# Kernel optimization log

Hardware: AMD Instinct MI355X
Metric: run time of the kernel (lower is better)

## Reference

```python
import jax, jax.numpy as jnp
import numpy as np

RADIUS = 5          # box-filter radius -> 11x11 kernel
TEMP = 0.5          # multinomial temperature
NSAMP = 5           # sampling_num
EPS = 1e-6
BN_EPS = 1e-5


def _conv(x, w, stride=1, padding=0, groups=1):
    return jax.lax.conv_general_dilated(
        x, w, window_strides=(stride, stride),
        padding=[(padding, padding), (padding, padding)],
        feature_group_count=groups,
        dimension_numbers=("NCHW", "OIHW", "NCHW"))


def custom_conv(x, w, key, stride=1, padding=0):
    """conv2d with cosine-activation regularization (bias=False path)."""
    B = x.shape[0]
    Cout = w.shape[0]
    # all-ones 'norm' conv on x*x
    x_norm = jnp.sqrt(_conv(x * x, jnp.ones_like(w), stride, padding))
    y = _conv(x, w, stride, padding)
    w_norm = jnp.sqrt(jnp.sum(w * w, axis=(1, 2, 3)))  # per-out-channel Frobenius norm
    cosine = y / (w_norm[None, :, None, None] + EPS) / (x_norm + EPS)
    # 11x11 depthwise box filter
    k = 2 * RADIUS + 1
    dw = jnp.ones((Cout, 1, k, k), x.dtype)
    cosine_mean = _conv(cosine, dw, 1, RADIUS, groups=Cout) / (k * k)
    H, W = cosine.shape[2], cosine.shape[3]
    # multinomial(NSAMP, exp(cosine/TEMP)) counts, no_grad in original
    logits = jax.lax.stop_gradient(cosine).reshape(B, Cout, H * W) / TEMP
    idx = jax.random.categorical(key, logits, axis=-1, shape=(NSAMP, B, Cout))
    bi = jnp.broadcast_to(jnp.arange(B)[None, :, None], (NSAMP, B, Cout))
    ci = jnp.broadcast_to(jnp.arange(Cout)[None, None, :], (NSAMP, B, Cout))
    mask = jnp.zeros((B, Cout, H * W), x.dtype).at[bi, ci, idx].add(1.0)
    cm = cosine_mean.reshape(B, Cout, H * W)
    act = ((mask * cm).sum(-1) / mask.sum(-1)).mean()
    return y, act


def batchnorm(x, g, b):
    # training-mode batch statistics (biased variance), like nn.BatchNorm2d
    m = x.mean(axis=(0, 2, 3), keepdims=True)
    v = x.var(axis=(0, 2, 3), keepdims=True)
    return (x - m) / jnp.sqrt(v + BN_EPS) * g[None, :, None, None] + b[None, :, None, None]


def setup_inputs() -> dict:
    key = jax.random.key(0)
    ks = jax.random.split(key, 10)
    x = jax.random.normal(ks[0], (16, 256, 56, 56), jnp.float32)
    w1 = jax.random.normal(ks[1], (64, 256, 1, 1), jnp.float32) * 0.05
    w2 = jax.random.normal(ks[2], (64, 64, 3, 3), jnp.float32) * 0.05
    w3 = jax.random.normal(ks[3], (256, 64, 1, 1), jnp.float32) * 0.05
    g1 = 1.0 + 0.05 * jax.random.normal(ks[4], (64,), jnp.float32)
    b1 = 0.05 * jax.random.normal(ks[5], (64,), jnp.float32)
    g2 = 1.0 + 0.05 * jax.random.normal(ks[6], (64,), jnp.float32)
    b2 = 0.05 * jax.random.normal(ks[7], (64,), jnp.float32)
    g3 = 1.0 + 0.05 * jax.random.normal(ks[8], (256,), jnp.float32)
    b3 = 0.05 * jax.random.normal(ks[9], (256,), jnp.float32)
    return {"x": x, "w1": w1, "w2": w2, "w3": w3,
            "g1": g1, "b1": b1, "g2": g2, "b2": b2, "g3": g3, "b3": b3}


def reference(x, w1, w2, w3, g1, b1, g2, b2, g3, b3):
    k0, k1, k2 = jax.random.split(jax.random.key(42), 3)
    acc = jnp.asarray(0.0, x.dtype)
    out, a = custom_conv(x, w1, k0)           # conv1x1
    acc = acc + a
    out = jax.nn.relu(batchnorm(out, g1, b1))
    out, a = custom_conv(out, w2, k1, padding=1)  # conv3x3, stride 1
    acc = acc + a
    out = jax.nn.relu(batchnorm(out, g2, b2))
    out, a = custom_conv(out, w3, k2)         # conv1x1 expand
    acc = acc + a
    out = batchnorm(out, g3, b3)
    out = jax.nn.relu(out + x)                # identity shortcut (downsample=None)
    return out, acc
```

## Files before the change

### kernel.cpp

```cpp
#include <hip/hip_runtime.h>
#include <stdint.h>
#include <math.h>

#define HW 3136
#define NPIX 50176

typedef __attribute__((ext_vector_type(8))) short bf16x8;
typedef __attribute__((ext_vector_type(4))) float f32x4;
#define MFMA16(a, b, c) __builtin_amdgcn_mfma_f32_16x16x32_bf16(a, b, c, 0, 0, 0)

__device__ __forceinline__ unsigned short f2bf(float f) {
  unsigned u = __float_as_uint(f);
  u = (u + 0x7fffu + ((u >> 16) & 1u)) >> 16;
  return (unsigned short)u;
}
__device__ __forceinline__ unsigned pk2(float a, float b) {
  return (unsigned)f2bf(a) | ((unsigned)f2bf(b) << 16);
}
__device__ __forceinline__ float bf2f(unsigned short h) {
  return __uint_as_float(((unsigned)h) << 16);
}

#define ROTL32(v, r) __builtin_rotateleft32((uint32_t)(v), (r))

__host__ __device__ inline void threefry2x32(uint32_t k0, uint32_t k1,
                                             uint32_t x0, uint32_t x1,
                                             uint32_t& o0, uint32_t& o1) {
  uint32_t k2 = k0 ^ k1 ^ 0x1BD11BDAu;
  x0 += k0; x1 += k1;
  x0 += x1; x1 = ROTL32(x1, 13); x1 ^= x0;
  x0 += x1; x1 = ROTL32(x1, 15); x1 ^= x0;
  x0 += x1; x1 = ROTL32(x1, 26); x1 ^= x0;
  x0 += x1; x1 = ROTL32(x1, 6);  x1 ^= x0;
  x0 += k1; x1 += k2 + 1u;
  x0 += x1; x1 = ROTL32(x1, 17); x1 ^= x0;
  x0 += x1; x1 = ROTL32(x1, 29); x1 ^= x0;
  x0 += x1; x1 = ROTL32(x1, 16); x1 ^= x0;
  x0 += x1; x1 = ROTL32(x1, 24); x1 ^= x0;
  x0 += k2; x1 += k0 + 2u;
  x0 += x1; x1 = ROTL32(x1, 13); x1 ^= x0;
  x0 += x1; x1 = ROTL32(x1, 15); x1 ^= x0;
  x0 += x1; x1 = ROTL32(x1, 26); x1 ^= x0;
  x0 += x1; x1 = ROTL32(x1, 6);  x1 ^= x0;
  x0 += k0; x1 += k1 + 3u;
  x0 += x1; x1 = ROTL32(x1, 17); x1 ^= x0;
  x0 += x1; x1 = ROTL32(x1, 29); x1 ^= x0;
  x0 += x1; x1 = ROTL32(x1, 16); x1 ^= x0;
  x0 += x1; x1 = ROTL32(x1, 24); x1 ^= x0;
  x0 += k1; x1 += k2 + 4u;
  x0 += x1; x1 = ROTL32(x1, 13); x1 ^= x0;
  x0 += x1; x1 = ROTL32(x1, 15); x1 ^= x0;
  x0 += x1; x1 = ROTL32(x1, 26); x1 ^= x0;
  x0 += x1; x1 = ROTL32(x1, 6);  x1 ^= x0;
  x0 += k2; x1 += k0 + 5u;
  o0 = x0; o1 = x1;
}

#define TF5_R(r)                                            \
  _Pragma("unroll") for (int i = 0; i < 5; ++i) {           \
    x0[i] += x1[i]; x1[i] = ROTL32(x1[i], r) ^ x0[i];       \
  }
#define TF5_INJ(a, b)                                       \
  _Pragma("unroll") for (int i = 0; i < 5; ++i) {           \
    x0[i] += (a); x1[i] += (b);                             \
  }
__device__ __forceinline__ void threefry5(uint32_t k0, uint32_t k1,
    const uint32_t xa[5], const uint32_t xb[5], uint32_t oa[5], uint32_t ob[5]) {
  uint32_t k2 = k0 ^ k1 ^ 0x1BD11BDAu;
  uint32_t x0[5], x1[5];
  #pragma unroll
  for (int i = 0; i < 5; ++i) { x0[i] = xa[i] + k0; x1[i] = xb[i] + k1; }
  TF5_R(13) TF5_R(15) TF5_R(26) TF5_R(6)  TF5_INJ(k1, k2 + 1u)
  TF5_R(17) TF5_R(29) TF5_R(16) TF5_R(24) TF5_INJ(k2, k0 + 2u)
  TF5_R(13) TF5_R(15) TF5_R(26) TF5_R(6)  TF5_INJ(k0, k1 + 3u)
  TF5_R(17) TF5_R(29) TF5_R(16) TF5_R(24) TF5_INJ(k1, k2 + 4u)
  TF5_R(13) TF5_R(15) TF5_R(26) TF5_R(6)  TF5_INJ(k2, k0 + 5u)
  #pragma unroll
  for (int i = 0; i < 5; ++i) { oa[i] = x0[i]; ob[i] = x1[i]; }
}

#define NLN2F -0.6931471805599453f
#define NEG2LOG2E -2.8853900817779268f
__device__ __forceinline__ float exp_draw(uint32_t bits) {
  float u = __uint_as_float((bits >> 9) | 0x3f800000u) - 1.0f;
  u = fmaxf(u, 1.17549435e-38f);
  return NLN2F * __log2f(u);
}

__global__ void wprep_k(const float* __restrict__ w1, const float* __restrict__ w2,
                        const float* __restrict__ w3, float* __restrict__ invwn,
                        unsigned short* __restrict__ W1b, unsigned short* __restrict__ W2tb,
                        unsigned short* __restrict__ W3b) {
  int i = blockIdx.x * 256 + threadIdx.x;
  if (i < 16384) {
    W1b[i] = f2bf(w1[i]);
  } else if (i < 53248) {
    int o = i - 16384;
    int co = o / 576, r = o % 576, tap = r >> 6, ci = r & 63;
    W2tb[o] = f2bf(w2[co * 576 + ci * 9 + tap]);
  } else if (i < 69632) {
    int o = i - 53248;
    W3b[o] = f2bf(w3[o]);
  } else {
    int t = i - 69632;
    if (t < 64) {
      float s = 0.f;
      for (int k = 0; k < 256; k++) { float v = w1[t * 256 + k]; s = fmaf(v, v, s); }
      invwn[t] = 1.0f / (sqrtf(s) + 1e-6f);
    } else if (t < 128) {
      int c = t - 64; float s = 0.f;
      for (int k = 0; k < 576; k++) { float v = w2[c * 576 + k]; s = fmaf(v, v, s); }
      invwn[t] = 1.0f / (sqrtf(s) + 1e-6f);
    } else if (t < 384) {
      int c = t - 128; float s = 0.f;
      for (int k = 0; k < 64; k++) { float v = w3[c * 64 + k]; s = fmaf(v, v, s); }
      invwn[t] = 1.0f / (sqrtf(s) + 1e-6f);
    }
  }
}

__global__ __launch_bounds__(256) void bn_fin(const float* __restrict__ Sp,
    const float* __restrict__ Qp, const float* __restrict__ g,
    const float* __restrict__ b, float* __restrict__ sc, float* __restrict__ sh,
    int nblk) {
  const int c = blockIdx.x, tid = threadIdx.x;
  const float* rs = Sp + (size_t)c * nblk;
  const float* rq = Qp + (size_t)c * nblk;
  float s = 0.f, q = 0.f;
  for (int i = tid; i < nblk; i += 256) { s += rs[i]; q += rq[i]; }
  #pragma unroll
  for (int o = 32; o; o >>= 1) { s += __shfl_xor(s, o); q += __shfl_xor(q, o); }
  __shared__ float S[4], Q[4];
  int lane = tid & 63, wave = tid >> 6;
  if (lane == 0) { S[wave] = s; Q[wave] = q; }
  __syncthreads();
  if (tid == 0) {
    float st = S[0] + S[1] + S[2] + S[3];
    float qt = Q[0] + Q[1] + Q[2] + Q[3];
    float mean = st * (1.0f / (float)NPIX);
    float var = qt * (1.0f / (float)NPIX) - mean * mean;
    float sv = g[c] / sqrtf(var + 1e-5f);
    sc[c] = sv; sh[c] = b[c] - mean * sv;
  }
}

__global__ __launch_bounds__(256) void conv1_mfma(
    const float* __restrict__ X, const unsigned short* __restrict__ Wb,
    const float* __restrict__ invwn, unsigned short* __restrict__ Y1,
    unsigned short* __restrict__ CS, float* __restrict__ Sp, float* __restrict__ Qp) {
#define ST1 264
#define NB1 784
  __shared__ __align__(16) unsigned short bq[64 * ST1];
  __shared__ float sqp[4][64];
  __shared__ float ixn[64];
  const int p0 = blockIdx.x * 64, b = blockIdx.y;
  const int bid = b * 49 + blockIdx.x;
  const int tid = threadIdx.x;
  const int lane = tid & 63, wave = tid >> 6;
  const int m = lane & 15, quad = lane >> 4;
  const int co0 = wave * 16;
  const float* Xb = X + (size_t)b * 256 * HW + p0;

  bf16x8 afr[8];
  const unsigned short* wrow = Wb + (co0 + m) * 256 + quad * 8;
  #pragma unroll
  for (int k = 0; k < 8; ++k) afr[k] = *(const bf16x8*)(wrow + k * 32);

  {
    const int px = tid & 63, rg = tid >> 6;
    float sq = 0.f;
    #pragma unroll
    for (int it = 0; it < 16; ++it) {
      int ci = rg * 64 + it * 4;
      float v0 = Xb[(size_t)(ci + 0) * HW + px];
      float v1 = Xb[(size_t)(ci + 1) * HW + px];
      float v2 = Xb[(size_t)(ci + 2) * HW + px];
      float v3 = Xb[(size_t)(ci + 3) * HW + px];
      sq += v0 * v0 + v1 * v1 + v2 * v2 + v3 * v3;
      *(uint2*)&bq[px * ST1 + ci] = make_uint2(pk2(v0, v1), pk2(v2, v3));
    }
    sqp[rg][px] = sq;
  }
  __syncthreads();
  if (tid < 64)
    ixn[tid] = 1.0f / (sqrtf(sqp[0][tid] + sqp[1][tid] + sqp[2][tid] + sqp[3][tid]) + 1e-6f);
  __syncthreads();

  f32x4 acc[4];
  #pragma unroll
  for (int nt = 0; nt < 4; ++nt) acc[nt] = (f32x4)0.f;
  #pragma unroll
  for (int nt = 0; nt < 4; ++nt) {
    const unsigned short* brow = &bq[(nt * 16 + m) * ST1 + quad * 8];
    #pragma unroll
    for (int k = 0; k < 8; ++k) {
      bf16x8 bfrag = *(const bf16x8*)(brow + k * 32);
      acc[nt] = MFMA16(afr[k], bfrag, acc[nt]);
    }
  }

  float s[4] = {0, 0, 0, 0}, q[4] = {0, 0, 0, 0};
  #pragma unroll
  for (int nt = 0; nt < 4; ++nt) {
    int px = nt * 16 + m;
    size_t bp = (size_t)b * HW + p0 + px;
    float ix = ixn[px];
    *(uint2*)&Y1[bp * 64 + co0 + quad * 4] =
        make_uint2(pk2(acc[nt][0], acc[nt][1]), pk2(acc[nt][2], acc[nt][3]));
    #pragma unroll
    for (int r = 0; r < 4; ++r) {
      int co = co0 + quad * 4 + r;
      float v = acc[nt][r];
      CS[((size_t)b * 64 + co) * HW + p0 + px] = f2bf(v * invwn[co] * ix);
      s[r] += v; q[r] = fmaf(v, v, q[r]);
    }
  }
  #pragma unroll
  for (int r = 0; r < 4; ++r) {
    float ss = s[r], qq = q[r];
    #pragma unroll
    for (int o = 8; o; o >>= 1) { ss += __shfl_xor(ss, o); qq += __shfl_xor(qq, o); }
    if (m == 0) {
      int co = co0 + quad * 4 + r;
      Sp[(size_t)co * NB1 + bid] = ss; Qp[(size_t)co * NB1 + bid] = qq;
    }
  }
#undef NB1
#undef ST1
}

__global__ __launch_bounds__(256) void chansum_px(const unsigned short* __restrict__ Y1,
    const float* __restrict__ sc, const float* __restrict__ sh,
    float* __restrict__ part) {
  int g = blockIdx.x * 256 + threadIdx.x;
  const unsigned short* row = Y1 + (size_t)g * 64;
  float s = 0.f;
  #pragma unroll
  for (int j = 0; j < 8; ++j) {
    uint4 d = *(const uint4*)(row + j * 8);
    unsigned dd[4] = {d.x, d.y, d.z, d.w};
    #pragma unroll
    for (int e = 0; e < 4; ++e) {
      int c = j * 8 + e * 2;
      float v0 = fmaxf(0.f, fmaf(bf2f((unsigned short)(dd[e] & 0xffff)), sc[c], sh[c]));
      float v1 = fmaxf(0.f, fmaf(bf2f((unsigned short)(dd[e] >> 16)), sc[c + 1], sh[c + 1]));
      s = fmaf(v0, v0, s); s = fmaf(v1, v1, s);
    }
  }
  part[g] = s;
}

__global__ __launch_bounds__(256) void box3inv(const float* __restrict__ part,
                                               float* __restrict__ out) {
  int g = blockIdx.x * 256 + threadIdx.x;
  int b = g / HW, p = g - b * HW;
  int y = p / 56, x = p % 56;
  float tot = 0.f;
  for (int dy = -1; dy <= 1; dy++) {
    int yy = y + dy; if (yy < 0 || yy >= 56) continue;
    for (int dx = -1; dx <= 1; dx++) {
      int xx = x + dx; if (xx < 0 || xx >= 56) continue;
      tot += part[b * HW + yy * 56 + xx];
    }
  }
  out[g] = 1.0f / (sqrtf(tot) + 1e-6f);
}

__global__ __launch_bounds__(256) void conv2_mfma(
    const unsigned short* __restrict__ Y1, const unsigned short* __restrict__ W2tb,
    const float* __restrict__ invwn, const float* __restrict__ ixn2,
    const float* __restrict__ sc1, const float* __restrict__ sh1,
    unsigned short* __restrict__ Y2, unsigned short* __restrict__ CS,
    float* __restrict__ Sp, float* __restrict__ Qp) {
#define STW 72
#define NB2 896
  __shared__ __align__(16) unsigned short ts[3 * 66 * STW];
  __shared__ float scl[64], shl[64];
  const int h = blockIdx.x, b = blockIdx.y;
  const int bid = b * 56 + h;
  const int tid = threadIdx.x;
  const int lane = tid & 63, wave = tid >> 6;
  const int m = lane & 15, quad = lane >> 4;
  const int co0 = wave * 16;
  if (tid < 64) { scl[tid] = sc1[tid]; shl[tid] = sh1[tid]; }

  bf16x8 afr[18];
  #pragma unroll
  for (int ks = 0; ks < 18; ++ks)
    afr[ks] = *(const bf16x8*)(W2tb + (co0 + m) * 576 + ks * 32 + quad * 8);
  __syncthreads();

  for (int l = tid; l < 6336; l += 256) {
    int cp = l & 31, cc = (l >> 5) % 66, dy = l / 2112;
    int yy = h - 1 + dy, xx = cc - 1;
    unsigned pkv = 0u;
    if (yy >= 0 && yy < 56 && xx >= 0 && xx < 56) {
      unsigned d = *(const unsigned*)&Y1[((size_t)b * HW + yy * 56 + xx) * 64 + cp * 2];
      float v0 = bf2f((unsigned short)(d & 0xffff));
      float v1 = bf2f((unsigned short)(d >> 16));
      v0 = fmaxf(0.f, fmaf(v0, scl[cp * 2], shl[cp * 2]));
      v1 = fmaxf(0.f, fmaf(v1, scl[cp * 2 + 1], shl[cp * 2 + 1]));
      pkv = pk2(v0, v1);
    }
    *(unsigned*)&ts[(dy * 66 + cc) * STW + cp * 2] = pkv;
  }
  __syncthreads();

  f32x4 acc[4];
  #pragma unroll
  for (int nt = 0; nt < 4; ++nt) acc[nt] = (f32x4)0.f;
  #pragma unroll
  for (int nt = 0; nt < 4; ++nt) {
    #pragma unroll
    for (int ks = 0; ks < 18; ++ks) {
      int tap = ks >> 1, half = ks & 1;
      int dy = tap / 3, dx = tap % 3;
      bf16x8 bfrag = *(const bf16x8*)&ts[(dy * 66 + nt * 16 + m + dx) * STW + half * 32 + quad * 8];
      acc[nt] = MFMA16(afr[ks], bfrag, acc[nt]);
    }
  }

  float s[4] = {0, 0, 0, 0}, q[4] = {0, 0, 0, 0};
  #pragma unroll
  for (int nt = 0; nt < 4; ++nt) {
    int px = nt * 16 + m;
    bool valid = px < 56;
    int pix = h * 56 + px;
    if (valid) {
      float ix = ixn2[b * HW + pix];
      size_t bp = (size_t)b * HW + pix;
      *(uint2*)&Y2[bp * 64 + co0 + quad * 4] =
          make_uint2(pk2(acc[nt][0], acc[nt][1]), pk2(acc[nt][2], acc[nt][3]));
      #pragma unroll
      for (int r = 0; r < 4; ++r) {
        int co = co0 + quad * 4 + r;
        CS[((size_t)b * 64 + co) * HW + pix] = f2bf(acc[nt][r] * invwn[co] * ix);
      }
    }
    #pragma unroll
    for (int r = 0; r < 4; ++r) {
      float v = valid ? acc[nt][r] : 0.f;
      s[r] += v; q[r] = fmaf(v, v, q[r]);
    }
  }
  #pragma unroll
  for (int r = 0; r < 4; ++r) {
    float ss = s[r], qq = q[r];
    #pragma unroll
    for (int o = 8; o; o >>= 1) { ss += __shfl_xor(ss, o); qq += __shfl_xor(qq, o); }
    if (m == 0) {
      int co = co0 + quad * 4 + r;
      Sp[(size_t)co * NB2 + bid] = ss; Qp[(size_t)co * NB2 + bid] = qq;
    }
  }
#undef NB2
#undef STW
}

__global__ __launch_bounds__(256) void conv3_mfma(
    const unsigned short* __restrict__ Y2, const unsigned short* __restrict__ W3b,
    const float* __restrict__ invwn,
    const float* __restrict__ sc2, const float* __restrict__ sh2,
    unsigned short* __restrict__ Y3, unsigned short* __restrict__ CS,
    float* __restrict__ Sp, float* __restrict__ Qp) {
#define ST3 72
#define NB3 784
  __shared__ __align__(16) unsigned short bq[64 * ST3];
  __shared__ float scl[64], shl[64], sqp[4][64], ixn[64];
  const int p0 = blockIdx.x * 64, b = blockIdx.y;
  const int bid = b * 49 + blockIdx.x;
  const int tid = threadIdx.x;
  const int lane = tid & 63, wave = tid >> 6;
  const int m = lane & 15, quad = lane >> 4;
  const int co0 = wave * 64;
  if (tid < 64) { scl[tid] = sc2[tid]; shl[tid] = sh2[tid]; }

  bf16x8 afr[4][2];
  #pragma unroll
  for (int mt = 0; mt < 4; ++mt)
    #pragma unroll
    for (int k = 0; k < 2; ++k)
      afr[mt][k] = *(const bf16x8*)(W3b + (co0 + mt * 16 + m) * 64 + k * 32 + quad * 8);
  __syncthreads();

  {
    const int cp = tid & 31, pxg = tid >> 5;
    #pragma unroll
    for (int it = 0; it < 8; ++it) {
      int px = pxg * 8 + it;
      unsigned d = *(const unsigned*)&Y2[((size_t)b * HW + p0 + px) * 64 + cp * 2];
      float v0 = bf2f((unsigned short)(d & 0xffff));
      float v1 = bf2f((unsigned short)(d >> 16));
      v0 = fmaxf(0.f, fmaf(v0, scl[cp * 2], shl[cp * 2]));
      v1 = fmaxf(0.f, fmaf(v1, scl[cp * 2 + 1], shl[cp * 2 + 1]));
      *(unsigned*)&bq[px * ST3 + cp * 2] = pk2(v0, v1);
    }
  }
  __syncthreads();
  {
    const int px = tid & 63, hh = tid >> 6;
    const unsigned short* row = &bq[px * ST3 + hh * 16];
    float sq = 0.f;
    #pragma unroll
    for (int e = 0; e < 16; ++e) { float v = bf2f(row[e]); sq = fmaf(v, v, sq); }
    sqp[hh][px] = sq;
  }
  __syncthreads();
  if (tid < 64)
    ixn[tid] = 1.0f / (sqrtf(sqp[0][tid] + sqp[1][tid] + sqp[2][tid] + sqp[3][tid]) + 1e-6f);
  __syncthreads();

  f32x4 acc[4][4];
  #pragma unroll
  for (int mt = 0; mt < 4; ++mt)
    #pragma unroll
    for (int nt = 0; nt < 4; ++nt) acc[mt][nt] = (f32x4)0.f;
  #pragma unroll
  for (int nt = 0; nt < 4; ++nt) {
    const unsigned short* brow = &bq[(nt * 16 + m) * ST3 + quad * 8];
    bf16x8 b0 = *(const bf16x8*)(brow);
    bf16x8 b1 = *(const bf16x8*)(brow + 32);
    #pragma unroll
    for (int mt = 0; mt < 4; ++mt) {
      acc[mt][nt] = MFMA16(afr[mt][0], b0, acc[mt][nt]);
      acc[mt][nt] = MFMA16(afr[mt][1], b1, acc[mt][nt]);
    }
  }

  #pragma unroll
  for (int mt = 0; mt < 4; ++mt) {
    float s[4] = {0, 0, 0, 0}, q[4] = {0, 0, 0, 0};
    #pragma unroll
    for (int nt = 0; nt < 4; ++nt) {
      int px = nt * 16 + m;
      float ix = ixn[px];
      #pragma unroll
      for (int r = 0; r < 4; ++r) {
        int co = co0 + mt * 16 + quad * 4 + r;
        float v = acc[mt][nt][r];
        size_t off = ((size_t)b * 256 + co) * HW + p0 + px;
        Y3[off] = f2bf(v);
        CS[off] = f2bf(v * invwn[co] * ix);
        s[r] += v; q[r] = fmaf(v, v, q[r]);
      }
    }
    #pragma unroll
    for (int r = 0; r < 4; ++r) {
      float ss = s[r], qq = q[r];
      #pragma unroll
      for (int o = 8; o; o >>= 1) { ss += __shfl_xor(ss, o); qq += __shfl_xor(qq, o); }
      if (m == 0) {
        int co = co0 + mt * 16 + quad * 4 + r;
        Sp[(size_t)co * NB3 + bid] = ss; Qp[(size_t)co * NB3 + bid] = qq;
      }
    }
  }
#undef NB3
#undef ST3
}

template <int NT>
__global__ __launch_bounds__(NT) void sample5_k(const unsigned short* __restrict__ CS,
    float* __restrict__ acc, uint32_t key0, uint32_t key1, int BC, float scale) {
  const int u = blockIdx.x;
  const int v = u + (BC >> 1);
  const uint32_t sC = (uint32_t)BC * (uint32_t)HW;
  const uint32_t halfn = sC * 2u + (sC >> 1);
  const unsigned short* rowU = CS + (size_t)u * HW;
  const unsigned short* rowV = CS + (size_t)v * HW;
  const int tid = threadIdx.x;
  const int lane = tid & 63;

  __shared__ unsigned kmin[10];
  __shared__ float wsum[10];
  if (tid < 10) { kmin[tid] = 0xFFFFFFFFu; wsum[tid] = 0.f; }

  unsigned bk[10];
  #pragma unroll
  for (int k = 0; k < 10; ++k) bk[k] = 0xFFFFFFFFu;

  const uint32_t baseU0 = (uint32_t)u * (uint32_t)HW;
  const uint32_t baseV0 = (uint32_t)v * (uint32_t)HW;
  for (int p = tid; p < HW; p += NT) {
    float wu = __builtin_amdgcn_exp2f(bf2f(rowU[p]) * NEG2LOG2E);
    float wv = __builtin_amdgcn_exp2f(bf2f(rowV[p]) * NEG2LOG2E);
    uint32_t eU = baseU0 + (uint32_t)p;
    uint32_t eV = baseV0 + (uint32_t)p;
    uint32_t xa[5] = {eU, eU + sC, eU + 2 * sC, eV, eV + sC};
    uint32_t xb[5] = {eU + halfn, eU + sC + halfn, eU + 2 * sC + halfn,
                      eV + halfn, eV + sC + halfn};
    uint32_t oa[5], ob[5];
    threefry5(key0, key1, xa, xb, oa, ob);
    uint32_t wds[10] = {oa[0], oa[1], oa[2], ob[3], ob[4],
                        oa[3], oa[4], ob[0], ob[1], ob[2]};
    #pragma unroll
    for (int k = 0; k < 10; ++k) {
      float s = exp_draw(wds[k]) * (k < 5 ? wu : wv);
      unsigned key = (__float_as_uint(s) & 0xFFFFF000u) | (unsigned)p;
      bk[k] = bk[k] < key ? bk[k] : key;
    }
  }

  __syncthreads();
  #pragma unroll
  for (int k = 0; k < 10; ++k) {
    unsigned kv = bk[k];
    #pragma unroll
    for (int o = 32; o; o >>= 1) {
      unsigned ov = __shfl_xor(kv, o);
      kv = kv < ov ? kv : ov;
    }
    if (lane == 0) atomicMin(&kmin[k], kv);
  }
  __syncthreads();

  for (int idx = tid; idx < 1210; idx += NT) {
    int win = idx / 121, j = idx - win * 121;
    int bidx = (int)(kmin[win] & 0xFFFu);
    int py = bidx / 56, px = bidx % 56;
    int yy = py + j / 11 - 5, xx = px + j % 11 - 5;
    if (yy >= 0 && yy < 56 && xx >= 0 && xx < 56) {
      const unsigned short* row = (win < 5) ? rowU : rowV;
      atomicAdd(&wsum[win], bf2f(row[yy * 56 + xx]));
    }
  }
  __syncthreads();
  if (tid == 0) {
    float t = 0.f;
    #pragma unroll
    for (int k = 0; k < 10; ++k) t += wsum[k];
    atomicAdd(acc, t * scale);
  }
}

__global__ __launch_bounds__(256) void final_k(const unsigned short* __restrict__ Y3,
    const float* __restrict__ X, const float* __restrict__ sc,
    const float* __restrict__ sh, const float* __restrict__ acc,
    float* __restrict__ out) {
  size_t i4 = (size_t)blockIdx.x * 256 + threadIdx.x;
  if (i4 == 0) out[12845056] = acc[0];
  size_t i = i4 * 4;
  int c = (int)((i / HW) % 256);
  float a = sc[c], d = sh[c];
  uint2 yd = *(const uint2*)&Y3[i];
  float4 xv = *(const float4*)&X[i];
  float4 r;
  r.x = fmaxf(0.f, fmaf(bf2f((unsigned short)(yd.x & 0xffff)), a, d) + xv.x);
  r.y = fmaxf(0.f, fmaf(bf2f((unsigned short)(yd.x >> 16)),    a, d) + xv.y);
  r.z = fmaxf(0.f, fmaf(bf2f((unsigned short)(yd.y & 0xffff)), a, d) + xv.z);
  r.w = fmaxf(0.f, fmaf(bf2f((unsigned short)(yd.y >> 16)),    a, d) + xv.w);
  *(float4*)&out[i] = r;
}

extern "C" void kernel_launch(void* const* d_in, const int* in_sizes, int n_in,
                              void* d_out, int out_size, void* d_ws, size_t ws_size,
                              hipStream_t stream) {
  (void)in_sizes; (void)n_in; (void)out_size; (void)ws_size;
  const float* x  = (const float*)d_in[0];
  const float* w1 = (const float*)d_in[1];
  const float* w2 = (const float*)d_in[2];
  const float* w3 = (const float*)d_in[3];
  const float* g1 = (const float*)d_in[4];
  const float* b1 = (const float*)d_in[5];
  const float* g2 = (const float*)d_in[6];
  const float* b2 = (const float*)d_in[7];
  const float* g3 = (const float*)d_in[8];
  const float* b3 = (const float*)d_in[9];
  float* out = (float*)d_out;
  float* ws = (float*)d_ws;

  size_t o = 0;
  unsigned short* y3b  = (unsigned short*)(ws + o); o += 6422528;
  unsigned short* cos3 = (unsigned short*)(ws + o); o += 6422528;
  unsigned short* CSb  = (unsigned short*)(ws + o); o += 1605632;
  unsigned short* y1b  = (unsigned short*)(ws + o); o += 1605632;
  unsigned short* y2b  = (unsigned short*)(ws + o); o += 1605632;
  unsigned short* W1b  = (unsigned short*)(ws + o); o += 8192;
  unsigned short* W2tb = (unsigned short*)(ws + o); o += 18432;
  unsigned short* W3b  = (unsigned short*)(ws + o); o += 8192;
  float* part = ws + o; o += NPIX;
  float* ixn2 = ws + o; o += NPIX;
  float* invwn = ws + o; o += 384;
  float* Sp1 = ws + o; o += 64 * 784;   float* Qp1 = ws + o; o += 64 * 784;
  float* Sp2 = ws + o; o += 64 * 896;   float* Qp2 = ws + o; o += 64 * 896;
  float* Sp3 = ws + o; o += 256 * 784;  float* Qp3 = ws + o; o += 256 * 784;
  float* acc = ws + o; o += 1;
  float* sc1 = ws + o; o += 64;  float* sh1 = ws + o; o += 64;
  float* sc2 = ws + o; o += 64;  float* sh2 = ws + o; o += 64;
  float* sc3 = ws + o; o += 256; float* sh3 = ws + o; o += 256;

  hipMemsetAsync(acc, 0, sizeof(float), stream);

  uint32_t A0, B0, A1, B1, A2, B2;
  threefry2x32(0u, 42u, 0u, 3u, A0, B0);
  threefry2x32(0u, 42u, 1u, 4u, A1, B1);
  threefry2x32(0u, 42u, 2u, 5u, A2, B2);

  const float scale64  = 1.0f / (121.0f * 5.0f * 1024.0f);
  const float scale256 = 1.0f / (121.0f * 5.0f * 4096.0f);

  wprep_k<<<274, 256, 0, stream>>>(w1, w2, w3, invwn, W1b, W2tb, W3b);

  conv1_mfma<<<dim3(49, 16), 256, 0, stream>>>(x, W1b, invwn, y1b, CSb, Sp1, Qp1);
  bn_fin<<<64, 256, 0, stream>>>(Sp1, Qp1, g1, b1, sc1, sh1, 784);
  sample5_k<512><<<512, 512, 0, stream>>>(CSb, acc, A0, A1, 1024, scale64);

  chansum_px<<<196, 256, 0, stream>>>(y1b, sc1, sh1, part);
  box3inv<<<196, 256, 0, stream>>>(part, ixn2);
  conv2_mfma<<<dim3(56, 16), 256, 0, stream>>>(
      y1b, W2tb, invwn + 64, ixn2, sc1, sh1, y2b, CSb, Sp2, Qp2);
  bn_fin<<<64, 256, 0, stream>>>(Sp2, Qp2, g2, b2, sc2, sh2, 896);
  sample5_k<512><<<512, 512, 0, stream>>>(CSb, acc, A2, B0, 1024, scale64);

  conv3_mfma<<<dim3(49, 16), 256, 0, stream>>>(
      y2b, W3b, invwn + 128, sc2, sh2, y3b, cos3, Sp3, Qp3);
  bn_fin<<<256, 256, 0, stream>>>(Sp3, Qp3, g3, b3, sc3, sh3, 784);
  sample5_k<256><<<2048, 256, 0, stream>>>(cos3, acc, B1, B2, 4096, scale256);
  final_k<<<12544, 256, 0, stream>>>(y3b, x, sc3, sh3, acc, out);
}
```

Before: 379.5 us.

## Fuse multinomial sampling blocks into following conv and final kernels

Each sampling kernel is folded into the next heavy kernel as extra interleaved blocks, so sampling of stage N runs alongside the conv of stage N+1 and the final elementwise pass. Stage 2 gets a second cosine buffer so it does not overwrite stage 1 while those are still being read, with a serial fallback when the workspace is too small. Sampling drops from 512 to 256 threads per block, and a tiny kernel now writes the accumulated scalar. The aim is to remove launch gaps and fill idle CUs, at the cost of uneven block durations and extra index arithmetic.

```diff
diff --git a/kernel.cpp b/kernel.cpp
--- a/kernel.cpp
+++ b/kernel.cpp
@@ -4,6 +4,8 @@
 
 #define HW 3136
 #define NPIX 50176
+
+__device__ __forceinline__ int min_i(int a, int b) { return a < b ? a : b; }
 
 typedef __attribute__((ext_vector_type(8))) short bf16x8;
 typedef __attribute__((ext_vector_type(4))) float f32x4;
@@ -87,6 +89,77 @@
   return NLN2F * __log2f(u);
 }
 
+__device__ void sample5_body(const unsigned short* __restrict__ CS,
+    float* __restrict__ acc, uint32_t key0, uint32_t key1, int BC, float scale,
+    int u, unsigned* kmin, float* wsum) {
+  const int v = u + (BC >> 1);
+  const uint32_t sC = (uint32_t)BC * (uint32_t)HW;
+  const uint32_t halfn = sC * 2u + (sC >> 1);
+  const unsigned short* rowU = CS + (size_t)u * HW;
+  const unsigned short* rowV = CS + (size_t)v * HW;
+  const int tid = threadIdx.x;
+  const int lane = tid & 63;
+
+  if (tid < 10) { kmin[tid] = 0xFFFFFFFFu; wsum[tid] = 0.f; }
+
+  unsigned bk[10];
+  #pragma unroll
+  for (int k = 0; k < 10; ++k) bk[k] = 0xFFFFFFFFu;
+
+  const uint32_t baseU0 = (uint32_t)u * (uint32_t)HW;
+  const uint32_t baseV0 = (uint32_t)v * (uint32_t)HW;
+  for (int p = tid; p < HW; p += 256) {
+    float wu = __builtin_amdgcn_exp2f(bf2f(rowU[p]) * NEG2LOG2E);
+    float wv = __builtin_amdgcn_exp2f(bf2f(rowV[p]) * NEG2LOG2E);
+    uint32_t eU = baseU0 + (uint32_t)p;
+    uint32_t eV = baseV0 + (uint32_t)p;
+    uint32_t xa[5] = {eU, eU + sC, eU + 2 * sC, eV, eV + sC};
+    uint32_t xb[5] = {eU + halfn, eU + sC + halfn, eU + 2 * sC + halfn,
+                      eV + halfn, eV + sC + halfn};
+    uint32_t oa[5], ob[5];
+    threefry5(key0, key1, xa, xb, oa, ob);
+    uint32_t wds[10] = {oa[0], oa[1], oa[2], ob[3], ob[4],
+                        oa[3], oa[4], ob[0], ob[1], ob[2]};
+    #pragma unroll
+    for (int k = 0; k < 10; ++k) {
+      float s = exp_draw(wds[k]) * (k < 5 ? wu : wv);
+      unsigned key = (__float_as_uint(s) & 0xFFFFF000u) | (unsigned)p;
+      bk[k] = bk[k] < key ? bk[k] : key;
+    }
+  }
+
+  __syncthreads();
+  #pragma unroll
+  for (int k = 0; k < 10; ++k) {
+    unsigned kv = bk[k];
+    #pragma unroll
+    for (int o = 32; o; o >>= 1) {
+      unsigned ov = __shfl_xor(kv, o);
+      kv = kv < ov ? kv : ov;
+    }
+    if (lane == 0) atomicMin(&kmin[k], kv);
+  }
+  __syncthreads();
+
+  for (int idx = tid; idx < 1210; idx += 256) {
+    int win = idx / 121, j = idx - win * 121;
+    int bidx = (int)(kmin[win] & 0xFFFu);
+    int py = bidx / 56, px = bidx % 56;
+    int yy = py + j / 11 - 5, xx = px + j % 11 - 5;
+    if (yy >= 0 && yy < 56 && xx >= 0 && xx < 56) {
+      const unsigned short* row = (win < 5) ? rowU : rowV;
+      atomicAdd(&wsum[win], bf2f(row[yy * 56 + xx]));
+    }
+  }
+  __syncthreads();
+  if (tid == 0) {
+    float t = 0.f;
+    #pragma unroll
+    for (int k = 0; k < 10; ++k) t += wsum[k];
+    atomicAdd(acc, t * scale);
+  }
+}
+
 __global__ void wprep_k(const float* __restrict__ w1, const float* __restrict__ w2,
                         const float* __restrict__ w3, float* __restrict__ invwn,
                         unsigned short* __restrict__ W1b, unsigned short* __restrict__ W2tb,
@@ -266,18 +339,28 @@
   out[g] = 1.0f / (sqrtf(tot) + 1e-6f);
 }
 
-__global__ __launch_bounds__(256) void conv2_mfma(
+__global__ __launch_bounds__(256) void conv2_samp_fused(
     const unsigned short* __restrict__ Y1, const unsigned short* __restrict__ W2tb,
     const float* __restrict__ invwn, const float* __restrict__ ixn2,
     const float* __restrict__ sc1, const float* __restrict__ sh1,
     unsigned short* __restrict__ Y2, unsigned short* __restrict__ CS,
-    float* __restrict__ Sp, float* __restrict__ Qp) {
+    float* __restrict__ Sp, float* __restrict__ Qp,
+    const unsigned short* __restrict__ CS1, float* __restrict__ accp,
+    uint32_t key0, uint32_t key1, float scale, int NS, int R) {
 #define STW 72
 #define NB2 896
   __shared__ __align__(16) unsigned short ts[3 * 66 * STW];
   __shared__ float scl[64], shl[64];
-  const int h = blockIdx.x, b = blockIdx.y;
-  const int bid = b * 56 + h;
+  const int g = blockIdx.x;
+  if (NS > 0 && (g % R) == 0 && (g / R) < NS) {
+    unsigned* kmin = (unsigned*)ts;
+    float* wsum = (float*)(ts + 32);
+    sample5_body(CS1, accp, key0, key1, 1024, scale, g / R, kmin, wsum);
+    return;
+  }
+  const int cb = g - min_i((g + R - 1) / R, NS);
+  const int h = cb % 56, b = cb / 56;
+  const int bid = cb;
   const int tid = threadIdx.x;
   const int lane = tid & 63, wave = tid >> 6;
   const int m = lane & 15, quad = lane >> 4;
@@ -357,18 +440,28 @@
 #undef STW
 }
 
-__global__ __launch_bounds__(256) void conv3_mfma(
+__global__ __launch_bounds__(256) void conv3_samp_fused(
     const unsigned short* __restrict__ Y2, const unsigned short* __restrict__ W3b,
     const float* __restrict__ invwn,
     const float* __restrict__ sc2, const float* __restrict__ sh2,
     unsigned short* __restrict__ Y3, unsigned short* __restrict__ CS,
-    float* __restrict__ Sp, float* __restrict__ Qp) {
+    float* __restrict__ Sp, float* __restrict__ Qp,
+    const unsigned short* __restrict__ CS2, float* __restrict__ accp,
+    uint32_t key0, uint32_t key1, float scale, int NS, int R) {
 #define ST3 72
 #define NB3 784
   __shared__ __align__(16) unsigned short bq[64 * ST3];
   __shared__ float scl[64], shl[64], sqp[4][64], ixn[64];
-  const int p0 = blockIdx.x * 64, b = blockIdx.y;
-  const int bid = b * 49 + blockIdx.x;
+  const int g = blockIdx.x;
+  if (NS > 0 && (g % R) == 0 && (g / R) < NS) {
+    unsigned* kmin = (unsigned*)bq;
+    float* wsum = (float*)(bq + 32);
+    sample5_body(CS2, accp, key0, key1, 1024, scale, g / R, kmin, wsum);
+    return;
+  }
+  const int cb = g - min_i((g + R - 1) / R, NS);
+  const int p0 = (cb % 49) * 64, b = cb / 49;
+  const int bid = cb;
   const int tid = threadIdx.x;
   const int lane = tid & 63, wave = tid >> 6;
   const int m = lane & 15, quad = lane >> 4;
@@ -459,86 +552,21 @@
 #undef ST3
 }
 
-template <int NT>
-__global__ __launch_bounds__(NT) void sample5_k(const unsigned short* __restrict__ CS,
-    float* __restrict__ acc, uint32_t key0, uint32_t key1, int BC, float scale) {
-  const int u = blockIdx.x;
-  const int v = u + (BC >> 1);
-  const uint32_t sC = (uint32_t)BC * (uint32_t)HW;
-  const uint32_t halfn = sC * 2u + (sC >> 1);
-  const unsigned short* rowU = CS + (size_t)u * HW;
-  const unsigned short* rowV = CS + (size_t)v * HW;
-  const int tid = threadIdx.x;
-  const int lane = tid & 63;
-
+__global__ __launch_bounds__(256) void final_samp_fused(
+    const unsigned short* __restrict__ Y3, const float* __restrict__ X,
+    const float* __restrict__ sc, const float* __restrict__ sh,
+    float* __restrict__ out, const unsigned short* __restrict__ CS3,
+    float* __restrict__ accp, uint32_t key0, uint32_t key1, float scale,
+    int NS, int R) {
   __shared__ unsigned kmin[10];
   __shared__ float wsum[10];
-  if (tid < 10) { kmin[tid] = 0xFFFFFFFFu; wsum[tid] = 0.f; }
-
-  unsigned bk[10];
-  #pragma unroll
-  for (int k = 0; k < 10; ++k) bk[k] = 0xFFFFFFFFu;
-
-  const uint32_t baseU0 = (uint32_t)u * (uint32_t)HW;
-  const uint32_t baseV0 = (uint32_t)v * (uint32_t)HW;
-  for (int p = tid; p < HW; p += NT) {
-    float wu = __builtin_amdgcn_exp2f(bf2f(rowU[p]) * NEG2LOG2E);
-    float wv = __builtin_amdgcn_exp2f(bf2f(rowV[p]) * NEG2LOG2E);
-    uint32_t eU = baseU0 + (uint32_t)p;
-    uint32_t eV = baseV0 + (uint32_t)p;
-    uint32_t xa[5] = {eU, eU + sC, eU + 2 * sC, eV, eV + sC};
-    uint32_t xb[5] = {eU + halfn, eU + sC + halfn, eU + 2 * sC + halfn,
-                      eV + halfn, eV + sC + halfn};
-    uint32_t oa[5], ob[5];
-    threefry5(key0, key1, xa, xb, oa, ob);
-    uint32_t wds[10] = {oa[0], oa[1], oa[2], ob[3], ob[4],
-                        oa[3], oa[4], ob[0], ob[1], ob[2]};
-    #pragma unroll
-    for (int k = 0; k < 10; ++k) {
-      float s = exp_draw(wds[k]) * (k < 5 ? wu : wv);
-      unsigned key = (__float_as_uint(s) & 0xFFFFF000u) | (unsigned)p;
-      bk[k] = bk[k] < key ? bk[k] : key;
-    }
-  }
-
-  __syncthreads();
-  #pragma unroll
-  for (int k = 0; k < 10; ++k) {
-    unsigned kv = bk[k];
-    #pragma unroll
-    for (int o = 32; o; o >>= 1) {
-      unsigned ov = __shfl_xor(kv, o);
-      kv = kv < ov ? kv : ov;
-    }
-    if (lane == 0) atomicMin(&kmin[k], kv);
-  }
-  __syncthreads();
-
-  for (int idx = tid; idx < 1210; idx += NT) {
-    int win = idx / 121, j = idx - win * 121;
-    int bidx = (int)(kmin[win] & 0xFFFu);
-    int py = bidx / 56, px = bidx % 56;
-    int yy = py + j / 11 - 5, xx = px + j % 11 - 5;
-    if (yy >= 0 && yy < 56 && xx >= 0 && xx < 56) {
-      const unsigned short* row = (win < 5) ? rowU : rowV;
-      atomicAdd(&wsum[win], bf2f(row[yy * 56 + xx]));
-    }
-  }
-  __syncthreads();
-  if (tid == 0) {
-    float t = 0.f;
-    #pragma unroll
-    for (int k = 0; k < 10; ++k) t += wsum[k];
-    atomicAdd(acc, t * scale);
-  }
-}
-
-__global__ __launch_bounds__(256) void final_k(const unsigned short* __restrict__ Y3,
-    const float* __restrict__ X, const float* __restrict__ sc,
-    const float* __restrict__ sh, const float* __restrict__ acc,
-    float* __restrict__ out) {
-  size_t i4 = (size_t)blockIdx.x * 256 + threadIdx.x;
-  if (i4 == 0) out[12845056] = acc[0];
+  const int g = blockIdx.x;
+  if (NS > 0 && (g % R) == 0 && (g / R) < NS) {
+    sample5_body(CS3, accp, key0, key1, 4096, scale, g / R, kmin, wsum);
+    return;
+  }
+  const int fb = g - min_i((g + R - 1) / R, NS);
+  size_t i4 = (size_t)fb * 256 + threadIdx.x;
   size_t i = i4 * 4;
   int c = (int)((i / HW) % 256);
   float a = sc[c], d = sh[c];
@@ -552,10 +580,14 @@
   *(float4*)&out[i] = r;
 }
 
+__global__ void acc_write_k(const float* __restrict__ accp, float* __restrict__ out) {
+  out[12845056] = accp[0];
+}
+
 extern "C" void kernel_launch(void* const* d_in, const int* in_sizes, int n_in,
                               void* d_out, int out_size, void* d_ws, size_t ws_size,
                               hipStream_t stream) {
-  (void)in_sizes; (void)n_in; (void)out_size; (void)ws_size;
+  (void)in_sizes; (void)n_in; (void)out_size;
   const float* x  = (const float*)d_in[0];
   const float* w1 = (const float*)d_in[1];
   const float* w2 = (const float*)d_in[2];
@@ -589,6 +621,9 @@
   float* sc2 = ws + o; o += 64;  float* sh2 = ws + o; o += 64;
   float* sc3 = ws + o; o += 256; float* sh3 = ws + o; o += 256;
 
+  const bool big = ws_size >= (o + 1605632) * sizeof(float);
+  unsigned short* CS2b = big ? (unsigned short*)(ws + o) : CSb;
+
   hipMemsetAsync(acc, 0, sizeof(float), stream);
 
   uint32_t A0, B0, A1, B1, A2, B2;
@@ -603,18 +638,38 @@
 
   conv1_mfma<<<dim3(49, 16), 256, 0, stream>>>(x, W1b, invwn, y1b, CSb, Sp1, Qp1);
   bn_fin<<<64, 256, 0, stream>>>(Sp1, Qp1, g1, b1, sc1, sh1, 784);
-  sample5_k<512><<<512, 512, 0, stream>>>(CSb, acc, A0, A1, 1024, scale64);
-
   chansum_px<<<196, 256, 0, stream>>>(y1b, sc1, sh1, part);
   box3inv<<<196, 256, 0, stream>>>(part, ixn2);
-  conv2_mfma<<<dim3(56, 16), 256, 0, stream>>>(
-      y1b, W2tb, invwn + 64, ixn2, sc1, sh1, y2b, CSb, Sp2, Qp2);
+
+  if (big) {
+    conv2_samp_fused<<<1408, 256, 0, stream>>>(
+        y1b, W2tb, invwn + 64, ixn2, sc1, sh1, y2b, CS2b, Sp2, Qp2,
+        CSb, acc, A0, A1, scale64, 512, 2);
+  } else {
+    conv2_samp_fused<<<512, 256, 0, stream>>>(
+        y1b, W2tb, invwn + 64, ixn2, sc1, sh1, y2b, CS2b, Sp2, Qp2,
+        CSb, acc, A0, A1, scale64, 512, 1);
+    conv2_samp_fused<<<896, 256, 0, stream>>>(
+        y1b, W2tb, invwn + 64, ixn2, sc1, sh1, y2b, CS2b, Sp2, Qp2,
+        CSb, acc, A0, A1, scale64, 0, 1);
+  }
   bn_fin<<<64, 256, 0, stream>>>(Sp2, Qp2, g2, b2, sc2, sh2, 896);
-  sample5_k<512><<<512, 512, 0, stream>>>(CSb, acc, A2, B0, 1024, scale64);
-
-  conv3_mfma<<<dim3(49, 16), 256, 0, stream>>>(
-      y2b, W3b, invwn + 128, sc2, sh2, y3b, cos3, Sp3, Qp3);
+
+  if (big) {
+    conv3_samp_fused<<<1296, 256, 0, stream>>>(
+        y2b, W3b, invwn + 128, sc2, sh2, y3b, cos3, Sp3, Qp3,
+        CS2b, acc, A2, B0, scale64, 512, 2);
+  } else {
+    conv3_samp_fused<<<512, 256, 0, stream>>>(
+        y2b, W3b, invwn + 128, sc2, sh2, y3b, cos3, Sp3, Qp3,
+        CS2b, acc, A2, B0, scale64, 512, 1);
+    conv3_samp_fused<<<784, 256, 0, stream>>>(
+        y2b, W3b, invwn + 128, sc2, sh2, y3b, cos3, Sp3, Qp3,
+        CS2b, acc, A2, B0, scale64, 0, 1);
+  }
   bn_fin<<<256, 256, 0, stream>>>(Sp3, Qp3, g3, b3, sc3, sh3, 784);
-  sample5_k<256><<<2048, 256, 0, stream>>>(cos3, acc, B1, B2, 4096, scale256);
-  final_k<<<12544, 256, 0, stream>>>(y3b, x, sc3, sh3, acc, out);
-}
+
+  final_samp_fused<<<14592, 256, 0, stream>>>(
+      y3b, x, sc3, sh3, out, cos3, acc, B1, B2, scale256, 2048, 2);
+  acc_write_k<<<1, 1, 0, stream>>>(acc, out);
+}
```

New measurement: 499.7 us. +31.7%, slower.

## Fuse third-stage sampling with final residual epilogue in one interleaved launch

Applied to the files above, without the earlier changes.

The third sampling kernel and the final BN+residual+ReLU elementwise kernel are merged into one grid. Every other block runs a sampling task and the remaining blocks do elementwise work, so compute-heavy RNG blocks overlap with bandwidth-bound epilogue blocks. The accumulator write moves to a tiny separate kernel at the end. The cost is one extra launch, plus sampling-path register pressure that may lower occupancy for the elementwise blocks.

```diff
diff --git a/kernel.cpp b/kernel.cpp
--- a/kernel.cpp
+++ b/kernel.cpp
@@ -4,6 +4,8 @@
 
 #define HW 3136
 #define NPIX 50176
+
+__device__ __forceinline__ int min_i(int a, int b) { return a < b ? a : b; }
 
 typedef __attribute__((ext_vector_type(8))) short bf16x8;
 typedef __attribute__((ext_vector_type(4))) float f32x4;
@@ -87,6 +89,86 @@
   return NLN2F * __log2f(u);
 }
 
+template <int NT>
+__device__ void sample5_body(const unsigned short* __restrict__ CS,
+    float* __restrict__ acc, uint32_t key0, uint32_t key1, int BC, float scale,
+    int u, unsigned* kmin, float* wsum) {
+  const int v = u + (BC >> 1);
+  const uint32_t sC = (uint32_t)BC * (uint32_t)HW;
+  const uint32_t halfn = sC * 2u + (sC >> 1);
+  const unsigned short* rowU = CS + (size_t)u * HW;
+  const unsigned short* rowV = CS + (size_t)v * HW;
+  const int tid = threadIdx.x;
+  const int lane = tid & 63;
+
+  if (tid < 10) { kmin[tid] = 0xFFFFFFFFu; wsum[tid] = 0.f; }
+
+  unsigned bk[10];
+  #pragma unroll
+  for (int k = 0; k < 10; ++k) bk[k] = 0xFFFFFFFFu;
+
+  const uint32_t baseU0 = (uint32_t)u * (uint32_t)HW;
+  const uint32_t baseV0 = (uint32_t)v * (uint32_t)HW;
+  for (int p = tid; p < HW; p += NT) {
+    float wu = __builtin_amdgcn_exp2f(bf2f(rowU[p]) * NEG2LOG2E);
+    float wv = __builtin_amdgcn_exp2f(bf2f(rowV[p]) * NEG2LOG2E);
+    uint32_t eU = baseU0 + (uint32_t)p;
+    uint32_t eV = baseV0 + (uint32_t)p;
+    uint32_t xa[5] = {eU, eU + sC, eU + 2 * sC, eV, eV + sC};
+    uint32_t xb[5] = {eU + halfn, eU + sC + halfn, eU + 2 * sC + halfn,
+                      eV + halfn, eV + sC + halfn};
+    uint32_t oa[5], ob[5];
+    threefry5(key0, key1, xa, xb, oa, ob);
+    uint32_t wds[10] = {oa[0], oa[1], oa[2], ob[3], ob[4],
+                        oa[3], oa[4], ob[0], ob[1], ob[2]};
+    #pragma unroll
+    for (int k = 0; k < 10; ++k) {
+      float s = exp_draw(wds[k]) * (k < 5 ? wu : wv);
+      unsigned key = (__float_as_uint(s) & 0xFFFFF000u) | (unsigned)p;
+      bk[k] = bk[k] < key ? bk[k] : key;
+    }
+  }
+
+  __syncthreads();
+  #pragma unroll
+  for (int k = 0; k < 10; ++k) {
+    unsigned kv = bk[k];
+    #pragma unroll
+    for (int o = 32; o; o >>= 1) {
+      unsigned ov = __shfl_xor(kv, o);
+      kv = kv < ov ? kv : ov;
+    }
+    if (lane == 0) atomicMin(&kmin[k], kv);
+  }
+  __syncthreads();
+
+  for (int idx = tid; idx < 1210; idx += NT) {
+    int win = idx / 121, j = idx - win * 121;
+    int bidx = (int)(kmin[win] & 0xFFFu);
+    int py = bidx / 56, px = bidx % 56;
+    int yy = py + j / 11 - 5, xx = px + j % 11 - 5;
+    if (yy >= 0 && yy < 56 && xx >= 0 && xx < 56) {
+      const unsigned short* row = (win < 5) ? rowU : rowV;
+      atomicAdd(&wsum[win], bf2f(row[yy * 56 + xx]));
+    }
+  }
+  __syncthreads();
+  if (tid == 0) {
+    float t = 0.f;
+    #pragma unroll
+    for (int k = 0; k < 10; ++k) t += wsum[k];
+    atomicAdd(acc, t * scale);
+  }
+}
+
+template <int NT>
+__global__ __launch_bounds__(NT) void sample5_k(const unsigned short* __restrict__ CS,
+    float* __restrict__ acc, uint32_t key0, uint32_t key1, int BC, float scale) {
+  __shared__ unsigned kmin[10];
+  __shared__ float wsum[10];
+  sample5_body<NT>(CS, acc, key0, key1, BC, scale, blockIdx.x, kmin, wsum);
+}
+
 __global__ void wprep_k(const float* __restrict__ w1, const float* __restrict__ w2,
                         const float* __restrict__ w3, float* __restrict__ invwn,
                         unsigned short* __restrict__ W1b, unsigned short* __restrict__ W2tb,
@@ -459,86 +541,21 @@
 #undef ST3
 }
 
-template <int NT>
-__global__ __launch_bounds__(NT) void sample5_k(const unsigned short* __restrict__ CS,
-    float* __restrict__ acc, uint32_t key0, uint32_t key1, int BC, float scale) {
-  const int u = blockIdx.x;
-  const int v = u + (BC >> 1);
-  const uint32_t sC = (uint32_t)BC * (uint32_t)HW;
-  const uint32_t halfn = sC * 2u + (sC >> 1);
-  const unsigned short* rowU = CS + (size_t)u * HW;
-  const unsigned short* rowV = CS + (size_t)v * HW;
-  const int tid = threadIdx.x;
-  const int lane = tid & 63;
-
+__global__ __launch_bounds__(256, 8) void final_samp_fused(
+    const unsigned short* __restrict__ Y3, const float* __restrict__ X,
+    const float* __restrict__ sc, const float* __restrict__ sh,
+    float* __restrict__ out, const unsigned short* __restrict__ CS3,
+    float* __restrict__ accp, uint32_t key0, uint32_t key1, float scale,
+    int NS, int R) {
   __shared__ unsigned kmin[10];
   __shared__ float wsum[10];
-  if (tid < 10) { kmin[tid] = 0xFFFFFFFFu; wsum[tid] = 0.f; }
-
-  unsigned bk[10];
-  #pragma unroll
-  for (int k = 0; k < 10; ++k) bk[k] = 0xFFFFFFFFu;
-
-  const uint32_t baseU0 = (uint32_t)u * (uint32_t)HW;
-  const uint32_t baseV0 = (uint32_t)v * (uint32_t)HW;
-  for (int p = tid; p < HW; p += NT) {
-    float wu = __builtin_amdgcn_exp2f(bf2f(rowU[p]) * NEG2LOG2E);
-    float wv = __builtin_amdgcn_exp2f(bf2f(rowV[p]) * NEG2LOG2E);
-    uint32_t eU = baseU0 + (uint32_t)p;
-    uint32_t eV = baseV0 + (uint32_t)p;
-    uint32_t xa[5] = {eU, eU + sC, eU + 2 * sC, eV, eV + sC};
-    uint32_t xb[5] = {eU + halfn, eU + sC + halfn, eU + 2 * sC + halfn,
-                      eV + halfn, eV + sC + halfn};
-    uint32_t oa[5], ob[5];
-    threefry5(key0, key1, xa, xb, oa, ob);
-    uint32_t wds[10] = {oa[0], oa[1], oa[2], ob[3], ob[4],
-                        oa[3], oa[4], ob[0], ob[1], ob[2]};
-    #pragma unroll
-    for (int k = 0; k < 10; ++k) {
-      float s = exp_draw(wds[k]) * (k < 5 ? wu : wv);
-      unsigned key = (__float_as_uint(s) & 0xFFFFF000u) | (unsigned)p;
-      bk[k] = bk[k] < key ? bk[k] : key;
-    }
-  }
-
-  __syncthreads();
-  #pragma unroll
-  for (int k = 0; k < 10; ++k) {
-    unsigned kv = bk[k];
-    #pragma unroll
-    for (int o = 32; o; o >>= 1) {
-      unsigned ov = __shfl_xor(kv, o);
-      kv = kv < ov ? kv : ov;
-    }
-    if (lane == 0) atomicMin(&kmin[k], kv);
-  }
-  __syncthreads();
-
-  for (int idx = tid; idx < 1210; idx += NT) {
-    int win = idx / 121, j = idx - win * 121;
-    int bidx = (int)(kmin[win] & 0xFFFu);
-    int py = bidx / 56, px = bidx % 56;
-    int yy = py + j / 11 - 5, xx = px + j % 11 - 5;
-    if (yy >= 0 && yy < 56 && xx >= 0 && xx < 56) {
-      const unsigned short* row = (win < 5) ? rowU : rowV;
-      atomicAdd(&wsum[win], bf2f(row[yy * 56 + xx]));
-    }
-  }
-  __syncthreads();
-  if (tid == 0) {
-    float t = 0.f;
-    #pragma unroll
-    for (int k = 0; k < 10; ++k) t += wsum[k];
-    atomicAdd(acc, t * scale);
-  }
-}
-
-__global__ __launch_bounds__(256) void final_k(const unsigned short* __restrict__ Y3,
-    const float* __restrict__ X, const float* __restrict__ sc,
-    const float* __restrict__ sh, const float* __restrict__ acc,
-    float* __restrict__ out) {
-  size_t i4 = (size_t)blockIdx.x * 256 + threadIdx.x;
-  if (i4 == 0) out[12845056] = acc[0];
+  const int g = blockIdx.x;
+  if ((g % R) == 0 && (g / R) < NS) {
+    sample5_body<256>(CS3, accp, key0, key1, 4096, scale, g / R, kmin, wsum);
+    return;
+  }
+  const int fb = g - min_i((g + R - 1) / R, NS);
+  size_t i4 = (size_t)fb * 256 + threadIdx.x;
   size_t i = i4 * 4;
   int c = (int)((i / HW) % 256);
   float a = sc[c], d = sh[c];
@@ -550,6 +567,10 @@
   r.z = fmaxf(0.f, fmaf(bf2f((unsigned short)(yd.y & 0xffff)), a, d) + xv.z);
   r.w = fmaxf(0.f, fmaf(bf2f((unsigned short)(yd.y >> 16)),    a, d) + xv.w);
   *(float4*)&out[i] = r;
+}
+
+__global__ void acc_write_k(const float* __restrict__ accp, float* __restrict__ out) {
+  out[12845056] = accp[0];
 }
 
 extern "C" void kernel_launch(void* const* d_in, const int* in_sizes, int n_in,
@@ -615,6 +636,8 @@
   conv3_mfma<<<dim3(49, 16), 256, 0, stream>>>(
       y2b, W3b, invwn + 128, sc2, sh2, y3b, cos3, Sp3, Qp3);
   bn_fin<<<256, 256, 0, stream>>>(Sp3, Qp3, g3, b3, sc3, sh3, 784);
-  sample5_k<256><<<2048, 256, 0, stream>>>(cos3, acc, B1, B2, 4096, scale256);
-  final_k<<<12544, 256, 0, stream>>>(y3b, x, sc3, sh3, acc, out);
-}
+
+  final_samp_fused<<<14592, 256, 0, stream>>>(
+      y3b, x, sc3, sh3, out, cos3, acc, B1, B2, scale256, 2048, 2);
+  acc_write_k<<<1, 1, 0, stream>>>(acc, out);
+}
```

Measured after the change: 451.6 us. +19.0%, slower.
